# Kernel optimization log

Measured on AMD Instinct MI355X. Metric: run time of the kernel, lower is better.

Reference implementation:

```python
import jax, jax.numpy as jnp
import numpy as np

N, C, H = 4096, 1024, 16
HD = C // H            # 64
DR = HD // 8           # 8 rope freqs per spatial axis


def setup_inputs() -> dict:
    key = jax.random.key(0)
    k1, k2, k3, k4, k5, k6 = jax.random.split(key, 6)
    x = jax.random.normal(k1, (N, C), dtype=jnp.float32)
    coords = jax.random.randint(k2, (N, 5), 0, 64, dtype=jnp.int32)  # [batch, t, h, w, z]
    w_qkv = jax.random.normal(k3, (3 * C, C), dtype=jnp.float32) / np.sqrt(C)
    w_out = jax.random.normal(k4, (C, C), dtype=jnp.float32) / np.sqrt(C)
    gamma_q = jnp.ones((H, HD), dtype=jnp.float32)
    gamma_k = jnp.ones((H, HD), dtype=jnp.float32)
    return {"x": x, "coords": coords, "w_qkv": w_qkv, "w_out": w_out,
            "gamma_q": gamma_q, "gamma_k": gamma_k}


def _rms_norm(t, gamma):
    # F.normalize(dim=-1) * gamma * sqrt(head_dim), computed in fp32
    t = t.astype(jnp.float32)
    nrm = jnp.linalg.norm(t, axis=-1, keepdims=True)
    return t / jnp.maximum(nrm, 1e-12) * gamma * np.float32(np.sqrt(HD))


def _rope_angles(coords):
    # freqs = 1/10000^(arange(DR)/HD); angles per axis (t,h,w,z), concat -> [N, 4*DR] = [N, HD/2]
    freqs = 1.0 / (10000.0 ** (jnp.arange(DR, dtype=jnp.float32) / HD))
    pos = coords[:, 1:].astype(jnp.float32)  # [N,4]
    ang = pos[:, :, None] * freqs[None, None, :]  # [N,4,DR]
    return ang.reshape(ang.shape[0], -1)  # [N, HD/2]


def _apply_rope(t, cos, sin):
    # t: [N,H,HD]; pairs (2i, 2i+1) rotated by angle[i]
    t2 = t.astype(jnp.float32).reshape(t.shape[0], t.shape[1], -1, 2)
    re = t2[..., 0] * cos - t2[..., 1] * sin
    im = t2[..., 0] * sin + t2[..., 1] * cos
    return jnp.stack([re, im], axis=-1).reshape(t.shape)


def reference(x, coords, w_qkv, w_out, gamma_q, gamma_k):
    n = x.shape[0]
    qkv = (x @ w_qkv.T).reshape(n, 3, H, HD)
    q, k, v = qkv[:, 0], qkv[:, 1], qkv[:, 2]  # [N,H,HD]
    q = _rms_norm(q, gamma_q)
    k = _rms_norm(k, gamma_k)
    ang = _rope_angles(coords)              # [N, HD/2]
    cos = jnp.cos(ang)[:, None, :]          # [N,1,HD/2] (broadcast over heads)
    sin = jnp.sin(ang)[:, None, :]
    q = _apply_rope(q, cos, sin)
    k = _apply_rope(k, cos, sin)
    scale = np.float32(1.0 / np.sqrt(HD))
    scores = jnp.einsum('nhd,mhd->hnm', q, k) * scale  # [H,N,N]
    attn = jax.nn.softmax(scores, axis=-1)
    out = jnp.einsum('hnm,mhd->nhd', attn, v).reshape(n, C)
    return out @ w_out.T
```

## Files before the change

### kernel.cpp

```cpp
#include <hip/hip_runtime.h>
#include <hip/hip_bf16.h>

typedef _Float16 half8 __attribute__((ext_vector_type(8)));
typedef _Float16 half4v __attribute__((ext_vector_type(4)));
typedef _Float16 half2 __attribute__((ext_vector_type(2)));
typedef float f32x4 __attribute__((ext_vector_type(4)));

constexpr int NT = 4096;
constexpr int CH = 1024;
constexpr int NH = 16;
constexpr int HD = 64;
constexpr int C3 = 3072;

#if __has_builtin(__builtin_amdgcn_exp2f)
#define EXP2(x) __builtin_amdgcn_exp2f(x)
#else
#define EXP2(x) exp2f(x)
#endif

#define GLOAD_LDS16(gp, lp) __builtin_amdgcn_global_load_lds( \
    (const __attribute__((address_space(1))) void*)(gp),      \
    (__attribute__((address_space(3))) void*)(lp), 16, 0, 0)

static __device__ inline half2 pk_f16(float a, float b) {
  auto r = __builtin_amdgcn_cvt_pkrtz(a, b);
  return *(half2*)&r;
}

__global__ __launch_bounds__(256) void cvt3_kernel(const float* __restrict__ a, int na4,
                                                   const float* __restrict__ b, int nb4,
                                                   const float* __restrict__ c, int nc4,
                                                   _Float16* __restrict__ oa,
                                                   _Float16* __restrict__ ob,
                                                   _Float16* __restrict__ oc) {
  int i = blockIdx.x * 256 + threadIdx.x;
  const float* src; _Float16* dst; int j = i;
  if (i < na4) { src = a; dst = oa; }
  else if (i < na4 + nb4) { src = b; dst = ob; j = i - na4; }
  else if (i < na4 + nb4 + nc4) { src = c; dst = oc; j = i - na4 - nb4; }
  else return;
  float4 v = ((const float4*)src)[j];
  half4v h;
  h[0] = (_Float16)v.x; h[1] = (_Float16)v.y; h[2] = (_Float16)v.z; h[3] = (_Float16)v.w;
  ((half4v*)dst)[j] = h;
}

__global__ __launch_bounds__(256) void rope_tab_kernel(const int* __restrict__ coords,
                                                       float2* __restrict__ csn) {
  int idx = blockIdx.x * 256 + threadIdx.x;
  int n = idx >> 5, j = idx & 31;
  float ang = (float)coords[n * 5 + 1 + (j >> 3)] * __expf(-(float)(j & 7) * 0.14391157f);
  csn[idx] = make_float2(cosf(ang), sinf(ang));
}

__global__ __launch_bounds__(512, 2) void gemm_qkv(const _Float16* __restrict__ A,
                                                   const _Float16* __restrict__ Bt,
                                                   const float2* __restrict__ csn,
                                                   const float* __restrict__ gq,
                                                   const float* __restrict__ gk,
                                                   _Float16* __restrict__ Qh,
                                                   _Float16* __restrict__ KF,
                                                   _Float16* __restrict__ VF) {
  __shared__ __align__(16) char smem[73728];
  auto As = (_Float16(*)[256][32])smem;
  auto Bs = (_Float16(*)[256][32])(smem + 32768);
  const int K = CH;
  const int tid = threadIdx.x;
  const int lane = tid & 63, w = tid >> 6;
  const int l15 = lane & 15, l4 = lane >> 4;
  int nwg = gridDim.x, cpx = nwg >> 3;
  int wg = (blockIdx.x & 7) * cpx + (blockIdx.x >> 3);
  const int nbx = NT / 256;
  const int bm = wg % nbx, bn = wg / nbx;
  const int m0 = bm * 256, n0 = bn * 256;
  const int wr = w >> 2, wc = w & 3;
  const int rb = w * 32;
  const int rl = lane >> 2;
  const int cb = (lane & 3) * 8;
  f32x4 acc[8][4] = {};
  auto stage = [&](int k0, int buf) {
    GLOAD_LDS16(A  + (size_t)(m0 + rb + rl) * K + k0 + cb,      &As[buf][rb][0]);
    GLOAD_LDS16(A  + (size_t)(m0 + rb + 16 + rl) * K + k0 + cb, &As[buf][rb + 16][0]);
    GLOAD_LDS16(Bt + (size_t)(n0 + rb + rl) * K + k0 + cb,      &Bs[buf][rb][0]);
    GLOAD_LDS16(Bt + (size_t)(n0 + rb + 16 + rl) * K + k0 + cb, &Bs[buf][rb + 16][0]);
  };
  auto compute = [&](int buf) {
    half8 af[8], bf[4];
#pragma unroll
    for (int mt = 0; mt < 8; ++mt) af[mt] = *(half8*)&As[buf][wr * 128 + mt * 16 + l15][l4 * 8];
#pragma unroll
    for (int nt = 0; nt < 4; ++nt) bf[nt] = *(half8*)&Bs[buf][wc * 64 + nt * 16 + l15][l4 * 8];
#pragma unroll
    for (int mt = 0; mt < 8; ++mt)
#pragma unroll
      for (int nt = 0; nt < 4; ++nt)
        acc[mt][nt] = __builtin_amdgcn_mfma_f32_16x16x32_f16(af[mt], bf[nt], acc[mt][nt], 0, 0, 0);
  };
  stage(0, 0);
  __syncthreads();
  for (int k0 = 0; k0 < K; k0 += 64) {
    stage(k0 + 32, 1);
    compute(0);
    __syncthreads();
    if (k0 + 64 < K) stage(k0 + 64, 0);
    compute(1);
    __syncthreads();
  }
  const int gc0 = n0 + wc * 64;
  const int sec = gc0 >> 10;
  const int h   = (gc0 & 1023) >> 6;
  _Float16* Lw = (_Float16*)(smem + w * 9216);
  float gmm[4];
  if (sec < 2) {
    const float* gm = (sec == 0) ? gq : gk;
#pragma unroll
    for (int nt = 0; nt < 4; ++nt) gmm[nt] = gm[h * 64 + nt * 16 + l15];
  }
  const float qsc = (sec == 0) ? 0.18033688f : 1.0f;
#pragma unroll
  for (int half = 0; half < 2; ++half) {
    const int K0 = m0 + wr * 128 + half * 64;
    if (sec < 2) {
#pragma unroll
      for (int mt = 0; mt < 4; ++mt)
#pragma unroll
        for (int r = 0; r < 4; ++r) {
          float ss = 0.f;
#pragma unroll
          for (int nt = 0; nt < 4; ++nt)
            ss += acc[half * 4 + mt][nt][r] * acc[half * 4 + mt][nt][r];
          ss += __shfl_xor(ss, 1); ss += __shfl_xor(ss, 2);
          ss += __shfl_xor(ss, 4); ss += __shfl_xor(ss, 8);
          float sc = 8.0f / fmaxf(sqrtf(ss), 1e-12f);
          int row = mt * 16 + l4 * 4 + r;
          int n = K0 + row;
#pragma unroll
          for (int nt = 0; nt < 4; ++nt) {
            float v = acc[half * 4 + mt][nt][r] * sc * gmm[nt];
            float2 cz = csn[n * 32 + nt * 8 + (l15 >> 1)];
            float p = __shfl_xor(v, 1);
            float o = ((l15 & 1) == 0) ? (v * cz.x - p * cz.y) : (p * cz.y + v * cz.x);
            Lw[row * 72 + nt * 16 + l15] = (_Float16)(o * qsc);
          }
        }
    } else {
#pragma unroll
      for (int mt = 0; mt < 4; ++mt)
#pragma unroll
        for (int r = 0; r < 4; ++r) {
          int row = mt * 16 + l4 * 4 + r;
#pragma unroll
          for (int nt = 0; nt < 4; ++nt)
            Lw[row * 72 + nt * 16 + l15] = (_Float16)acc[half * 4 + mt][nt][r];
        }
    }
    const int kb = K0 >> 6;
    if (sec == 0) {
#pragma unroll
      for (int i = 0; i < 8; ++i) {
        int row = i * 8 + (lane >> 3), col = (lane & 7) * 8;
        half8 vv = *(half8*)&Lw[row * 72 + col];
        *(half8*)(Qh + ((size_t)h * NT + K0 + row) * 64 + col) = vv;
      }
    } else if (sec == 1) {
      _Float16* base = KF + (size_t)h * NT * HD + (size_t)kb * 4096;
#pragma unroll
      for (int i = 0; i < 8; ++i) {
        int t = i >> 1, kk = i & 1;
        int i15 = lane & 15, ll4 = lane >> 4;
        int m = ((t >> 1) << 5) | ((i15 >> 2) << 3) | ((t & 1) << 2) | (i15 & 3);
        half8 vv = *(half8*)&Lw[m * 72 + kk * 32 + ll4 * 8];
        *(half8*)(base + (size_t)(((t * 2 + kk) * 64 + ll4 * 16 + i15) * 8)) = vv;
      }
    } else {
      _Float16* base = VF + (size_t)h * NT * HD + (size_t)kb * 4096;
#pragma unroll
      for (int i = 0; i < 8; ++i) {
        int t = i >> 1, kk = i & 1;
        int l15v = lane & 15, l4v = lane >> 4;
        half8 vv;
#pragma unroll
        for (int jj = 0; jj < 8; ++jj)
          vv[jj] = Lw[(kk * 32 + l4v * 8 + jj) * 72 + t * 16 + l15v];
        *(half8*)(base + (size_t)(((t * 2 + kk) * 64 + l4v * 16 + l15v) * 8)) = vv;
      }
    }
  }
}

template <typename OutT>
__global__ __launch_bounds__(256) void gemm_bt(const _Float16* __restrict__ A,
                                               const _Float16* __restrict__ Bt,
                                               OutT* __restrict__ Cc,
                                               int M, int Nn, int K, int nbx) {
  __shared__ _Float16 As[2][128][32];
  __shared__ _Float16 Bs[2][128][32];
  const int tid = threadIdx.x;
  const int lane = tid & 63, w = tid >> 6;
  const int l15 = lane & 15, l4 = lane >> 4;
  int nwg = gridDim.x, cpx = nwg >> 3;
  int wg = (blockIdx.x & 7) * cpx + (blockIdx.x >> 3);
  const int m0 = (wg % nbx) * 128, n0 = (wg / nbx) * 128;
  const int wr = w >> 1, wc = w & 1;
  const int rb = w * 32;
  const int rl = lane >> 2;
  const int cb = (lane & 3) * 8;
  f32x4 acc[4][4] = {};
  auto stage = [&](int k0, int buf) {
    GLOAD_LDS16(A  + (size_t)(m0 + rb + rl) * K + k0 + cb,      &As[buf][rb][0]);
    GLOAD_LDS16(A  + (size_t)(m0 + rb + 16 + rl) * K + k0 + cb, &As[buf][rb + 16][0]);
    GLOAD_LDS16(Bt + (size_t)(n0 + rb + rl) * K + k0 + cb,      &Bs[buf][rb][0]);
    GLOAD_LDS16(Bt + (size_t)(n0 + rb + 16 + rl) * K + k0 + cb, &Bs[buf][rb + 16][0]);
  };
  auto compute = [&](int buf) {
    half8 af[4], bf[4];
#pragma unroll
    for (int mt = 0; mt < 4; ++mt) af[mt] = *(half8*)&As[buf][wr * 64 + mt * 16 + l15][l4 * 8];
#pragma unroll
    for (int nt = 0; nt < 4; ++nt) bf[nt] = *(half8*)&Bs[buf][wc * 64 + nt * 16 + l15][l4 * 8];
#pragma unroll
    for (int mt = 0; mt < 4; ++mt)
#pragma unroll
      for (int nt = 0; nt < 4; ++nt)
        acc[mt][nt] = __builtin_amdgcn_mfma_f32_16x16x32_f16(af[mt], bf[nt], acc[mt][nt], 0, 0, 0);
  };
  stage(0, 0);
  __syncthreads();
  for (int k0 = 0; k0 < K; k0 += 64) {
    stage(k0 + 32, 1);
    compute(0);
    __syncthreads();
    if (k0 + 64 < K) stage(k0 + 64, 0);
    compute(1);
    __syncthreads();
  }
#pragma unroll
  for (int mt = 0; mt < 4; ++mt)
#pragma unroll
    for (int nt = 0; nt < 4; ++nt)
#pragma unroll
      for (int r = 0; r < 4; ++r) {
        int row = m0 + wr * 64 + mt * 16 + l4 * 4 + r;
        int col = n0 + wc * 64 + nt * 16 + l15;
        Cc[(size_t)row * Nn + col] = (OutT)acc[mt][nt][r];
      }
}

__global__ __launch_bounds__(256, 2) void attn_kernel(const _Float16* __restrict__ Qh,
                                                      const _Float16* __restrict__ KF,
                                                      const _Float16* __restrict__ VF,
                                                      _Float16* __restrict__ Oh) {
  __shared__ _Float16 KB[4096];
  __shared__ _Float16 VB[4096];
  const int tid = threadIdx.x, lane = tid & 63, w = tid >> 6;
  const int l15 = lane & 15, l4 = lane >> 4;
  int bid = blockIdx.x;
  int s = bid >> 3;
  int h = (bid & 7) * 2 + (s >> 5);
  int n0 = (s & 31) * 128;
  half8 qf[2][2];
#pragma unroll
  for (int qb = 0; qb < 2; ++qb)
#pragma unroll
    for (int kk = 0; kk < 2; ++kk)
      qf[qb][kk] = *(const half8*)(Qh + ((size_t)h * NT + n0 + w * 32 + qb * 16 + l15) * HD + kk * 32 + l4 * 8);
  f32x4 acc[2][4] = {};
  f32x4 acc5[2] = {};
  half8 of1 = {};
  if (l15 == 0) {
#pragma unroll
    for (int jq = 0; jq < 8; ++jq) of1[jq] = (_Float16)1.0f;
  }
  const _Float16* KFh = KF + (size_t)h * NT * HD + w * 512 + lane * 8;
  const _Float16* VFh = VF + (size_t)h * NT * HD + w * 512 + lane * 8;
  union U { half8 v; half2 p[4]; };
  for (int kb = 0; kb < 64; ++kb) {
    __syncthreads();
    {
      size_t g0 = (size_t)kb * 4096;
      GLOAD_LDS16(KFh + g0,        &KB[w * 512]);
      GLOAD_LDS16(KFh + g0 + 2048, &KB[2048 + w * 512]);
      GLOAD_LDS16(VFh + g0,        &VB[w * 512]);
      GLOAD_LDS16(VFh + g0 + 2048, &VB[2048 + w * 512]);
    }
    __syncthreads();
    f32x4 sv[2][4] = {};
    __builtin_amdgcn_s_setprio(1);
#pragma unroll
    for (int t = 0; t < 4; ++t)
#pragma unroll
      for (int kk = 0; kk < 2; ++kk) {
        half8 kf = *(half8*)&KB[(t * 2 + kk) * 512 + lane * 8];
        sv[0][t] = __builtin_amdgcn_mfma_f32_16x16x32_f16(kf, qf[0][kk], sv[0][t], 0, 0, 0);
        sv[1][t] = __builtin_amdgcn_mfma_f32_16x16x32_f16(kf, qf[1][kk], sv[1][t], 0, 0, 0);
      }
    __builtin_amdgcn_s_setprio(0);
    U u[2][2];
#pragma unroll
    for (int qb = 0; qb < 2; ++qb) {
      float e[4][4];
#pragma unroll
      for (int t = 0; t < 4; ++t)
#pragma unroll
        for (int r = 0; r < 4; ++r) e[t][r] = EXP2(sv[qb][t][r]);
      u[qb][0].p[0] = pk_f16(e[0][0], e[0][1]); u[qb][0].p[1] = pk_f16(e[0][2], e[0][3]);
      u[qb][0].p[2] = pk_f16(e[1][0], e[1][1]); u[qb][0].p[3] = pk_f16(e[1][2], e[1][3]);
      u[qb][1].p[0] = pk_f16(e[2][0], e[2][1]); u[qb][1].p[1] = pk_f16(e[2][2], e[2][3]);
      u[qb][1].p[2] = pk_f16(e[3][0], e[3][1]); u[qb][1].p[3] = pk_f16(e[3][2], e[3][3]);
    }
    __builtin_amdgcn_s_setprio(1);
#pragma unroll
    for (int t = 0; t < 4; ++t)
#pragma unroll
      for (int kk = 0; kk < 2; ++kk) {
        half8 vf = *(half8*)&VB[(t * 2 + kk) * 512 + lane * 8];
        acc[0][t] = __builtin_amdgcn_mfma_f32_16x16x32_f16(u[0][kk].v, vf, acc[0][t], 0, 0, 0);
        acc[1][t] = __builtin_amdgcn_mfma_f32_16x16x32_f16(u[1][kk].v, vf, acc[1][t], 0, 0, 0);
      }
    acc5[0] = __builtin_amdgcn_mfma_f32_16x16x32_f16(u[0][0].v, of1, acc5[0], 0, 0, 0);
    acc5[0] = __builtin_amdgcn_mfma_f32_16x16x32_f16(u[0][1].v, of1, acc5[0], 0, 0, 0);
    acc5[1] = __builtin_amdgcn_mfma_f32_16x16x32_f16(u[1][0].v, of1, acc5[1], 0, 0, 0);
    acc5[1] = __builtin_amdgcn_mfma_f32_16x16x32_f16(u[1][1].v, of1, acc5[1], 0, 0, 0);
    __builtin_amdgcn_s_setprio(0);
  }
#pragma unroll
  for (int qb = 0; qb < 2; ++qb) {
    float linv[4];
#pragma unroll
    for (int r = 0; r < 4; ++r) linv[r] = 1.0f / __shfl(acc5[qb][r], lane & 48);
#pragma unroll
    for (int t = 0; t < 4; ++t)
#pragma unroll
      for (int r = 0; r < 4; ++r) {
        int row = n0 + w * 32 + qb * 16 + l4 * 4 + r;
        Oh[(size_t)row * CH + h * HD + t * 16 + l15] = (_Float16)(acc[qb][t][r] * linv[r]);
      }
  }
}

extern "C" void kernel_launch(void* const* d_in, const int* in_sizes, int n_in,
                              void* d_out, int out_size, void* d_ws, size_t ws_size,
                              hipStream_t stream) {
  const float* x      = (const float*)d_in[0];
  const int*   coords = (const int*)d_in[1];
  const float* w_qkv  = (const float*)d_in[2];
  const float* w_out  = (const float*)d_in[3];
  const float* gq     = (const float*)d_in[4];
  const float* gk     = (const float*)d_in[5];
  float* out = (float*)d_out;

  char* ws = (char*)d_ws;
  size_t off = 0;
  auto alloc = [&](size_t bytes) { char* p = ws + off; off += bytes; return p; };
  _Float16* xh   = (_Float16*)alloc((size_t)NT * CH * 2);
  _Float16* wqh  = (_Float16*)alloc((size_t)C3 * CH * 2);
  _Float16* woh  = (_Float16*)alloc((size_t)CH * CH * 2);
  float2*   csn  = (float2*)alloc((size_t)NT * 32 * 8);
  _Float16* Qh   = (_Float16*)alloc((size_t)NT * CH * 2);
  _Float16* KFh  = (_Float16*)alloc((size_t)NT * CH * 2);
  _Float16* VFh  = (_Float16*)alloc((size_t)NT * CH * 2);
  _Float16* Oh   = (_Float16*)alloc((size_t)NT * CH * 2);
  if (off > ws_size) return;

  int na4 = NT * CH / 4, nb4 = C3 * CH / 4, nc4 = CH * CH / 4;
  cvt3_kernel<<<(na4 + nb4 + nc4) / 256, 256, 0, stream>>>(x, na4, w_qkv, nb4, w_out, nc4,
                                                           xh, wqh, woh);
  rope_tab_kernel<<<NT * 32 / 256, 256, 0, stream>>>(coords, csn);
  gemm_qkv<<<(NT / 256) * (C3 / 256), 512, 0, stream>>>(xh, wqh, csn, gq, gk, Qh, KFh, VFh);
  attn_kernel<<<NH * (NT / 128), 256, 0, stream>>>(Qh, KFh, VFh, Oh);
  gemm_bt<float><<<(NT / 128) * (CH / 128), 256, 0, stream>>>(Oh, woh, out, NT, CH, CH, NT / 128);
}
```

Baseline: 154.1 us.

## Keep two k-tiles in flight in GEMM loops with partial vmcnt waits

Both GEMM kernels now issue loads for the first two k-tiles up front. The main loop waits only until the older tile's four loads have landed (vmcnt(4)) instead of draining every load at each __syncthreads. This keeps one tile's global-to-LDS transfer overlapped with MFMA work on the other buffer. MFMA sections are also wrapped in s_setprio(1) to favour issuing matrix instructions. The risk is ordering: correctness depends on the hand-written waitcnt and barrier placement around the LDS buffer reuse.

```diff
diff --git a/kernel.cpp b/kernel.cpp
--- a/kernel.cpp
+++ b/kernel.cpp
@@ -21,6 +21,11 @@
 #define GLOAD_LDS16(gp, lp) __builtin_amdgcn_global_load_lds( \
     (const __attribute__((address_space(1))) void*)(gp),      \
     (__attribute__((address_space(3))) void*)(lp), 16, 0, 0)
+
+#define WAITCNT4 do { asm volatile("s_waitcnt vmcnt(4)" ::: "memory"); \
+                      __builtin_amdgcn_sched_barrier(0); } while (0)
+#define WAITCNT0 do { asm volatile("s_waitcnt vmcnt(0)" ::: "memory"); \
+                      __builtin_amdgcn_sched_barrier(0); } while (0)
 
 static __device__ inline half2 pk_f16(float a, float b) {
   auto r = __builtin_amdgcn_cvt_pkrtz(a, b);
@@ -90,22 +95,28 @@
     for (int mt = 0; mt < 8; ++mt) af[mt] = *(half8*)&As[buf][wr * 128 + mt * 16 + l15][l4 * 8];
 #pragma unroll
     for (int nt = 0; nt < 4; ++nt) bf[nt] = *(half8*)&Bs[buf][wc * 64 + nt * 16 + l15][l4 * 8];
+    __builtin_amdgcn_s_setprio(1);
 #pragma unroll
     for (int mt = 0; mt < 8; ++mt)
 #pragma unroll
       for (int nt = 0; nt < 4; ++nt)
         acc[mt][nt] = __builtin_amdgcn_mfma_f32_16x16x32_f16(af[mt], bf[nt], acc[mt][nt], 0, 0, 0);
+    __builtin_amdgcn_s_setprio(0);
   };
   stage(0, 0);
-  __syncthreads();
-  for (int k0 = 0; k0 < K; k0 += 64) {
-    stage(k0 + 32, 1);
-    compute(0);
-    __syncthreads();
-    if (k0 + 64 < K) stage(k0 + 64, 0);
-    compute(1);
-    __syncthreads();
-  }
+  stage(32, 1);
+  for (int k0 = 0; k0 < K - 32; k0 += 32) {
+    int buf = (k0 >> 5) & 1;
+    WAITCNT4;
+    __builtin_amdgcn_s_barrier();
+    compute(buf);
+    __builtin_amdgcn_s_barrier();
+    if (k0 + 64 < K) stage(k0 + 64, buf);
+  }
+  WAITCNT0;
+  __builtin_amdgcn_s_barrier();
+  compute(((K - 32) >> 5) & 1);
+  __builtin_amdgcn_s_barrier();
   const int gc0 = n0 + wc * 64;
   const int sec = gc0 >> 10;
   const int h   = (gc0 & 1023) >> 6;
@@ -218,22 +229,27 @@
     for (int mt = 0; mt < 4; ++mt) af[mt] = *(half8*)&As[buf][wr * 64 + mt * 16 + l15][l4 * 8];
 #pragma unroll
     for (int nt = 0; nt < 4; ++nt) bf[nt] = *(half8*)&Bs[buf][wc * 64 + nt * 16 + l15][l4 * 8];
+    __builtin_amdgcn_s_setprio(1);
 #pragma unroll
     for (int mt = 0; mt < 4; ++mt)
 #pragma unroll
       for (int nt = 0; nt < 4; ++nt)
         acc[mt][nt] = __builtin_amdgcn_mfma_f32_16x16x32_f16(af[mt], bf[nt], acc[mt][nt], 0, 0, 0);
+    __builtin_amdgcn_s_setprio(0);
   };
   stage(0, 0);
-  __syncthreads();
-  for (int k0 = 0; k0 < K; k0 += 64) {
-    stage(k0 + 32, 1);
-    compute(0);
-    __syncthreads();
-    if (k0 + 64 < K) stage(k0 + 64, 0);
-    compute(1);
-    __syncthreads();
-  }
+  stage(32, 1);
+  for (int k0 = 0; k0 < K - 32; k0 += 32) {
+    int buf = (k0 >> 5) & 1;
+    WAITCNT4;
+    __builtin_amdgcn_s_barrier();
+    compute(buf);
+    __builtin_amdgcn_s_barrier();
+    if (k0 + 64 < K) stage(k0 + 64, buf);
+  }
+  WAITCNT0;
+  __builtin_amdgcn_s_barrier();
+  compute(((K - 32) >> 5) & 1);
 #pragma unroll
   for (int mt = 0; mt < 4; ++mt)
 #pragma unroll
```

New measurement: 153.7 us. Within noise of the previous version (-0.3%).
